# Performance work log

Hardware: AMD Instinct MI355X
Metric: run time of the kernel (lower is better)

The kernel has to match this reference:

```python
import jax, jax.numpy as jnp
import numpy as np


def setup_inputs() -> dict:
    key = jax.random.key(0)
    k1, k2 = jax.random.split(key)
    B, H, W, C = 16, 128, 128, 192
    prv = jax.random.normal(k1, (B, H, W, C), dtype=jnp.float32)
    nxt = jax.random.normal(k2, (B, H, W, C), dtype=jnp.float32)
    return {"prv": prv, "nxt": nxt, "search_range": 4}


def reference(prv, nxt, search_range):
    # prv, nxt: [B, H, W, C] (NHWC). Output: [B, H, W, d*d] with d = 2r+1.
    r = int(search_range)
    d = 2 * r + 1
    # Zero-pad nxt by r on both spatial dims (matches ZeroPadding2D(r)).
    pad_nxt = jnp.pad(nxt, ((0, 0), (r, r), (r, r), (0, 0)))
    costs = []
    # Fixed small loop over d*d displacement offsets (81 for r=4); each
    # iteration is one fused multiply + channel-mean over the full tensor.
    for i0 in range(d):
        for j0 in range(d):
            roi = jax.lax.dynamic_slice(pad_nxt, (0, i0, j0, 0), prv.shape)
            costs.append(jnp.mean(prv * roi, axis=3))  # [B, H, W]
    return jnp.stack(costs, axis=3)  # [B, H, W, d*d], offsets in row-major (i0, j0) order
```

## Files before the change

### kernel.cpp

```cpp
#include <hip/hip_runtime.h>


typedef __attribute__((ext_vector_type(8))) short short8;
typedef __attribute__((ext_vector_type(4))) float float4v;

#define HH 128
#define WW 128
#define CC 192
#define BUFB 32768
#define GROWP 17
#define GWAVE (144 * GROWP)

static __device__ __forceinline__ unsigned int pk2(float lo, float hi) {
    unsigned int r;
    asm("v_cvt_pk_bf16_f32 %0, %1, %2" : "=v"(r) : "v"(lo), "v"(hi));
    return r;
}

static __device__ __forceinline__ short8 cvt8pk(const float* __restrict__ p) {
    float4v f0 = *reinterpret_cast<const float4v*>(p);
    float4v f1 = *reinterpret_cast<const float4v*>(p + 4);
    union { unsigned int u[4]; short8 s; } r;
    r.u[0] = pk2(f0[0], f0[1]);
    r.u[1] = pk2(f0[2], f0[3]);
    r.u[2] = pk2(f1[0], f1[1]);
    r.u[3] = pk2(f1[2], f1[3]);
    return r.s;
}

static __device__ __forceinline__ void gll16(const float* g, void* l) {
    __builtin_amdgcn_global_load_lds(
        (const __attribute__((address_space(1))) unsigned int*)g,
        (__attribute__((address_space(3))) unsigned int*)l,
        16, 0, 0);
}

__global__ __launch_bounds__(256, 2) void costvol_kernel(
    const float* __restrict__ prv,
    const float* __restrict__ nxt,
    float* __restrict__ out)
{
    const int tid  = threadIdx.x;
    const int lane = tid & 63;
    const int wv   = tid >> 6;
    const int m    = lane & 15;
    const int q    = lane >> 4;
    const int wr   = wv >> 1, wc = wv & 1;

    int bid = blockIdx.x + (blockIdx.y << 4) + (blockIdx.z << 8);
    bid = (bid & 7) * 512 + (bid >> 3);
    const int wt = bid & 15, ht = (bid >> 4) & 15, b = bid >> 8;
    const int h0 = ht * 8, w0 = wt * 8;

    const float* nxt_b = nxt + (size_t)b * HH * WW * CC;
    const float* prv_b = prv + (size_t)b * HH * WW * CC;

    __shared__ alignas(16) unsigned char smem[2 * BUFB];

    const int u32 = tid >> 3;
    const int jg  = tid & 7;
    const int jsw = jg ^ (u32 & 7);
    const int hcol = u32 & 15;
    const int dpar = u32 >> 4;
    const int wwg = w0 - 4 + hcol;
    const bool okw = (wwg >= 0) && (wwg < WW);
    const int wcl = wwg < 0 ? 0 : (wwg > WW - 1 ? WW - 1 : wwg);

    const float* gp[8];
    unsigned okmask = 0;
#pragma unroll
    for (int i = 0; i < 8; ++i) {
        int hh = h0 - 4 + 2 * i + dpar;
        bool ok = okw && (hh >= 0) && (hh < HH);
        int hcl = hh < 0 ? 0 : (hh > HH - 1 ? HH - 1 : hh);
        gp[i] = nxt_b + ((size_t)(hcl * WW + wcl)) * CC + jsw * 4;
        okmask |= (unsigned)ok << i;
    }
    const bool edge = (wt == 0) | (wt == 15) | (ht == 0) | (ht == 15);

    int roffA[9];
#pragma unroll
    for (int s = 0; s < 9; ++s) {
        int n  = s * 16 + m;
        int nr = n / 12, nc = n - nr * 12;
        int P  = (wr * 4 + nr) * 16 + (wc * 4 + nc);
        roffA[s] = (P * 128 + q * 32) ^ ((P & 7) << 4);
    }

    const int pr = m >> 2, pc = m & 3;
    const float* pbase =
        prv_b + ((size_t)(h0 + wr * 4 + pr) * WW + (w0 + wc * 4 + pc)) * CC + q * 8;
    short8 afrag[6];
#pragma unroll
    for (int kk = 0; kk < 6; ++kk) afrag[kk] = cvt8pk(pbase + kk * 32);

    unsigned char* ldsw = smem + wv * 1024;

#pragma unroll
    for (int i = 0; i < 8; ++i) gll16(gp[i],      ldsw + 0 * BUFB + i * 4096);
#pragma unroll
    for (int i = 0; i < 8; ++i) gll16(gp[i] + 32, ldsw + 1 * BUFB + i * 4096);
    __syncthreads();
    if (edge) {
#pragma unroll
        for (int i = 0; i < 8; ++i)
            if (!((okmask >> i) & 1u))
                *reinterpret_cast<float4v*>(smem + 0 * BUFB + i * 4096 + u32 * 128 + jg * 16)
                    = (float4v){0.f, 0.f, 0.f, 0.f};
    }
    asm volatile("s_waitcnt lgkmcnt(0)" ::: "memory");
    __builtin_amdgcn_sched_barrier(0);
    __builtin_amdgcn_s_barrier();
    __builtin_amdgcn_sched_barrier(0);
    asm volatile("" ::: "memory");

    float4v acc[9];
#pragma unroll
    for (int s = 0; s < 9; ++s) acc[s] = (float4v){0.f, 0.f, 0.f, 0.f};

#pragma unroll
    for (int kk = 0; kk < 6; ++kk) {
        const int rb = kk & 1;
        short8 a = afrag[kk];
#pragma unroll
        for (int s = 0; s < 9; ++s) {
            float4v f0 = *reinterpret_cast<const float4v*>(smem + rb * BUFB + roffA[s]);
            float4v f1 = *reinterpret_cast<const float4v*>(smem + rb * BUFB + (roffA[s] ^ 16));
            union { unsigned int u[4]; short8 s8; } fr;
            fr.u[0] = pk2(f0[0], f0[1]);
            fr.u[1] = pk2(f0[2], f0[3]);
            fr.u[2] = pk2(f1[0], f1[1]);
            fr.u[3] = pk2(f1[2], f1[3]);
            acc[s] = __builtin_amdgcn_mfma_f32_16x16x32_bf16(a, fr.s8, acc[s], 0, 0, 0);
        }
        __syncthreads();
        if (kk < 4) {
#pragma unroll
            for (int i = 0; i < 8; ++i)
                gll16(gp[i] + (kk + 2) * 32, ldsw + rb * BUFB + i * 4096);
        }
        if (kk < 5) {
            if (edge) {
                const int zb = (kk + 1) & 1;
#pragma unroll
                for (int i = 0; i < 8; ++i)
                    if (!((okmask >> i) & 1u))
                        *reinterpret_cast<float4v*>(smem + zb * BUFB + i * 4096 + u32 * 128 + jg * 16)
                            = (float4v){0.f, 0.f, 0.f, 0.f};
            }
            asm volatile("s_waitcnt lgkmcnt(0)" ::: "memory");
            __builtin_amdgcn_sched_barrier(0);
            __builtin_amdgcn_s_barrier();
            __builtin_amdgcn_sched_barrier(0);
            asm volatile("" ::: "memory");
        }
    }

    float* Gf = reinterpret_cast<float*>(smem);
    const int gbase = wv * GWAVE;
#pragma unroll
    for (int s = 0; s < 9; ++s) {
        int col = s * 16 + m;
#pragma unroll
        for (int r = 0; r < 4; ++r)
            Gf[gbase + col * GROWP + q * 4 + r] = acc[s][r];
    }
    __syncthreads();

    const float scale = 1.0f / 192.0f;
#pragma unroll
    for (int t = 0; t < 21; ++t) {
        int f = t * 256 + tid;
        if (f < 5184) {
            int p   = f / 81;
            int k   = f - p * 81;
            int i0  = k / 9, j0 = k - i0 * 9;
            int pr8 = p >> 3, pc8 = p & 7;
            int gw  = ((pr8 >> 2) << 1) | (pc8 >> 2);
            int pi  = ((pr8 & 3) << 2) | (pc8 & 3);
            int col = ((pr8 & 3) + i0) * 12 + ((pc8 & 3) + j0);
            float v = Gf[gw * GWAVE + col * GROWP + pi] * scale;
            out[((size_t)(b * HH + (h0 + pr8)) * WW + (w0 + pc8)) * 81 + k] = v;
        }
    }
}

extern "C" void kernel_launch(void* const* d_in, const int* in_sizes, int n_in,
                              void* d_out, int out_size, void* d_ws, size_t ws_size,
                              hipStream_t stream) {
    const float* prv = (const float*)d_in[0];
    const float* nxt = (const float*)d_in[1];
    float* out = (float*)d_out;
    dim3 grid(WW / 8, HH / 8, 16);
    dim3 block(256);
    hipLaunchKernelGGL(costvol_kernel, grid, block, 0, stream, prv, nxt, out);
}
```

Baseline: 435.7 us.

## Pre-convert nxt halo to bf16 in LDS via register staging, raise occupancy

Replaces direct global-to-LDS fp32 loads with per-thread register loads of one halo pixel, converted to bf16 and stored into a padded LDS layout, with zero-masking folded into the pack. MFMA B fragments then become a single 16-byte LDS read with no conversion. Each wave now computes 12 full 16-column tiles, including some redundant columns, to simplify indexing. LDS use shrinks enough to request four blocks per CU instead of two. The trade-off is extra MFMA work and more register pressure from the staging buffers.

```diff
diff --git a/kernel.cpp b/kernel.cpp
--- a/kernel.cpp
+++ b/kernel.cpp
@@ -3,11 +3,13 @@
 
 typedef __attribute__((ext_vector_type(8))) short short8;
 typedef __attribute__((ext_vector_type(4))) float float4v;
+typedef __attribute__((ext_vector_type(4))) unsigned int uint4v;
 
 #define HH 128
 #define WW 128
 #define CC 192
-#define BUFB 32768
+#define PSTR 80
+#define BUFB (256 * PSTR)
 #define GROWP 17
 #define GWAVE (144 * GROWP)
 
@@ -17,9 +19,7 @@
     return r;
 }
 
-static __device__ __forceinline__ short8 cvt8pk(const float* __restrict__ p) {
-    float4v f0 = *reinterpret_cast<const float4v*>(p);
-    float4v f1 = *reinterpret_cast<const float4v*>(p + 4);
+static __device__ __forceinline__ short8 cvt8r(float4v f0, float4v f1) {
     union { unsigned int u[4]; short8 s; } r;
     r.u[0] = pk2(f0[0], f0[1]);
     r.u[1] = pk2(f0[2], f0[3]);
@@ -28,14 +28,21 @@
     return r.s;
 }
 
-static __device__ __forceinline__ void gll16(const float* g, void* l) {
-    __builtin_amdgcn_global_load_lds(
-        (const __attribute__((address_space(1))) unsigned int*)g,
-        (__attribute__((address_space(3))) unsigned int*)l,
-        16, 0, 0);
+static __device__ __forceinline__ void cvt_store(unsigned char* dst,
+                                                 const float4v sv[8],
+                                                 unsigned wmask) {
+#pragma unroll
+    for (int g = 0; g < 4; ++g) {
+        uint4v w;
+        w.x = pk2(sv[2*g][0],   sv[2*g][1])   & wmask;
+        w.y = pk2(sv[2*g][2],   sv[2*g][3])   & wmask;
+        w.z = pk2(sv[2*g+1][0], sv[2*g+1][1]) & wmask;
+        w.w = pk2(sv[2*g+1][2], sv[2*g+1][3]) & wmask;
+        *reinterpret_cast<uint4v*>(dst + g * 16) = w;
+    }
 }
 
-__global__ __launch_bounds__(256, 2) void costvol_kernel(
+__global__ __launch_bounds__(256, 4) void costvol_kernel(
     const float* __restrict__ prv,
     const float* __restrict__ nxt,
     float* __restrict__ out)
@@ -57,113 +64,85 @@
 
     __shared__ alignas(16) unsigned char smem[2 * BUFB];
 
-    const int u32 = tid >> 3;
-    const int jg  = tid & 7;
-    const int jsw = jg ^ (u32 & 7);
-    const int hcol = u32 & 15;
-    const int dpar = u32 >> 4;
-    const int wwg = w0 - 4 + hcol;
-    const bool okw = (wwg >= 0) && (wwg < WW);
-    const int wcl = wwg < 0 ? 0 : (wwg > WW - 1 ? WW - 1 : wwg);
+    const int hr = tid >> 4, hcp = tid & 15;
+    const int gh = h0 - 4 + hr, gw_ = w0 - 4 + hcp;
+    const bool okp = (gh >= 0) && (gh < HH) && (gw_ >= 0) && (gw_ < WW);
+    const unsigned wmask = okp ? 0xFFFFFFFFu : 0u;
+    const int ghc = gh  < 0 ? 0 : (gh  > HH - 1 ? HH - 1 : gh);
+    const int gwc = gw_ < 0 ? 0 : (gw_ > WW - 1 ? WW - 1 : gw_);
+    const float* gpix = nxt_b + ((size_t)ghc * WW + gwc) * CC;
+    const int wbase = tid * PSTR;
 
-    const float* gp[8];
-    unsigned okmask = 0;
+    int roff[12];
 #pragma unroll
-    for (int i = 0; i < 8; ++i) {
-        int hh = h0 - 4 + 2 * i + dpar;
-        bool ok = okw && (hh >= 0) && (hh < HH);
-        int hcl = hh < 0 ? 0 : (hh > HH - 1 ? HH - 1 : hh);
-        gp[i] = nxt_b + ((size_t)(hcl * WW + wcl)) * CC + jsw * 4;
-        okmask |= (unsigned)ok << i;
-    }
-    const bool edge = (wt == 0) | (wt == 15) | (ht == 0) | (ht == 15);
+    for (int ls = 0; ls < 12; ++ls)
+        roff[ls] = ((wr * 4 + ls) * 16 + m) * PSTR + q * 16;
 
-    int roffA[9];
+    const float* pbase =
+        prv_b + ((size_t)(h0 + wr * 4 + (m >> 2)) * WW + (w0 + wc * 4 + (m & 3))) * CC + q * 8;
+
+    float4v ar0, ar1;
+    float4v sv[8];
+
+    ar0 = *reinterpret_cast<const float4v*>(pbase + 0);
+    ar1 = *reinterpret_cast<const float4v*>(pbase + 4);
 #pragma unroll
-    for (int s = 0; s < 9; ++s) {
-        int n  = s * 16 + m;
-        int nr = n / 12, nc = n - nr * 12;
-        int P  = (wr * 4 + nr) * 16 + (wc * 4 + nc);
-        roffA[s] = (P * 128 + q * 32) ^ ((P & 7) << 4);
-    }
-
-    const int pr = m >> 2, pc = m & 3;
-    const float* pbase =
-        prv_b + ((size_t)(h0 + wr * 4 + pr) * WW + (w0 + wc * 4 + pc)) * CC + q * 8;
-    short8 afrag[6];
+    for (int i = 0; i < 8; ++i)
+        sv[i] = *reinterpret_cast<const float4v*>(gpix + i * 4);
+    short8 a_cur = cvt8r(ar0, ar1);
+    cvt_store(smem + wbase, sv, wmask);
+    ar0 = *reinterpret_cast<const float4v*>(pbase + 32);
+    ar1 = *reinterpret_cast<const float4v*>(pbase + 36);
 #pragma unroll
-    for (int kk = 0; kk < 6; ++kk) afrag[kk] = cvt8pk(pbase + kk * 32);
-
-    unsigned char* ldsw = smem + wv * 1024;
-
-#pragma unroll
-    for (int i = 0; i < 8; ++i) gll16(gp[i],      ldsw + 0 * BUFB + i * 4096);
-#pragma unroll
-    for (int i = 0; i < 8; ++i) gll16(gp[i] + 32, ldsw + 1 * BUFB + i * 4096);
-    __syncthreads();
-    if (edge) {
-#pragma unroll
-        for (int i = 0; i < 8; ++i)
-            if (!((okmask >> i) & 1u))
-                *reinterpret_cast<float4v*>(smem + 0 * BUFB + i * 4096 + u32 * 128 + jg * 16)
-                    = (float4v){0.f, 0.f, 0.f, 0.f};
-    }
+    for (int i = 0; i < 8; ++i)
+        sv[i] = *reinterpret_cast<const float4v*>(gpix + 32 + i * 4);
     asm volatile("s_waitcnt lgkmcnt(0)" ::: "memory");
     __builtin_amdgcn_sched_barrier(0);
     __builtin_amdgcn_s_barrier();
     __builtin_amdgcn_sched_barrier(0);
-    asm volatile("" ::: "memory");
 
-    float4v acc[9];
+    float4v acc[12];
 #pragma unroll
-    for (int s = 0; s < 9; ++s) acc[s] = (float4v){0.f, 0.f, 0.f, 0.f};
+    for (int ls = 0; ls < 12; ++ls) acc[ls] = (float4v){0.f, 0.f, 0.f, 0.f};
 
 #pragma unroll
     for (int kk = 0; kk < 6; ++kk) {
-        const int rb = kk & 1;
-        short8 a = afrag[kk];
+        const int rb = (kk & 1) * BUFB;
 #pragma unroll
-        for (int s = 0; s < 9; ++s) {
-            float4v f0 = *reinterpret_cast<const float4v*>(smem + rb * BUFB + roffA[s]);
-            float4v f1 = *reinterpret_cast<const float4v*>(smem + rb * BUFB + (roffA[s] ^ 16));
-            union { unsigned int u[4]; short8 s8; } fr;
-            fr.u[0] = pk2(f0[0], f0[1]);
-            fr.u[1] = pk2(f0[2], f0[3]);
-            fr.u[2] = pk2(f1[0], f1[1]);
-            fr.u[3] = pk2(f1[2], f1[3]);
-            acc[s] = __builtin_amdgcn_mfma_f32_16x16x32_bf16(a, fr.s8, acc[s], 0, 0, 0);
-        }
-        __syncthreads();
-        if (kk < 4) {
-#pragma unroll
-            for (int i = 0; i < 8; ++i)
-                gll16(gp[i] + (kk + 2) * 32, ldsw + rb * BUFB + i * 4096);
+        for (int ls = 0; ls < 12; ++ls) {
+            short8 bf = *reinterpret_cast<const short8*>(smem + rb + roff[ls]);
+            acc[ls] = __builtin_amdgcn_mfma_f32_16x16x32_bf16(a_cur, bf, acc[ls], 0, 0, 0);
         }
         if (kk < 5) {
-            if (edge) {
-                const int zb = (kk + 1) & 1;
+            short8 a_nxt = cvt8r(ar0, ar1);
+            cvt_store(smem + ((kk + 1) & 1) * BUFB + wbase, sv, wmask);
+            if (kk < 4) {
+                ar0 = *reinterpret_cast<const float4v*>(pbase + (kk + 2) * 32);
+                ar1 = *reinterpret_cast<const float4v*>(pbase + (kk + 2) * 32 + 4);
 #pragma unroll
                 for (int i = 0; i < 8; ++i)
-                    if (!((okmask >> i) & 1u))
-                        *reinterpret_cast<float4v*>(smem + zb * BUFB + i * 4096 + u32 * 128 + jg * 16)
-                            = (float4v){0.f, 0.f, 0.f, 0.f};
+                    sv[i] = *reinterpret_cast<const float4v*>(gpix + (kk + 2) * 32 + i * 4);
             }
             asm volatile("s_waitcnt lgkmcnt(0)" ::: "memory");
             __builtin_amdgcn_sched_barrier(0);
             __builtin_amdgcn_s_barrier();
             __builtin_amdgcn_sched_barrier(0);
-            asm volatile("" ::: "memory");
+            a_cur = a_nxt;
         }
     }
 
+    __syncthreads();
     float* Gf = reinterpret_cast<float*>(smem);
     const int gbase = wv * GWAVE;
+    const int lc = m - wc * 4;
+    if (lc >= 0 && lc < 12) {
 #pragma unroll
-    for (int s = 0; s < 9; ++s) {
-        int col = s * 16 + m;
+        for (int ls = 0; ls < 12; ++ls) {
+            int col = ls * 12 + lc;
 #pragma unroll
-        for (int r = 0; r < 4; ++r)
-            Gf[gbase + col * GROWP + q * 4 + r] = acc[s][r];
+            for (int r = 0; r < 4; ++r)
+                Gf[gbase + col * GROWP + q * 4 + r] = acc[ls][r];
+        }
     }
     __syncthreads();
 
```

After: 474.4 us. +8.9%, slower.
